# Optimization experiments

Hardware: AMD Instinct MI355X
Metric: run time of the kernel (lower is better)

The kernel has to match this reference:

```python
import jax, jax.numpy as jnp
import numpy as np

Nu, Nd = 40000, 20000          # users, drugs
FIN, HID, H = 128, 256, 4      # input feat, hidden_dim, heads
D = HID // H                   # per-head dim (64)
HAN_OUT, HD = 64, 16           # HANConv out_channels, per-head dim
E, ER = 80000, 80000           # edges per relation (main / refined graph)


def _seg_softmax(a, seg, num):
    # segment softmax over destination index, stable
    m = jax.ops.segment_max(a, seg, num_segments=num)
    ex = jnp.exp(a - m[seg])
    s = jax.ops.segment_sum(ex, seg, num_segments=num)
    return ex / (s[seg] + 1e-16)


def setup_inputs():
    key = jax.random.key(0)
    ks = iter(jax.random.split(key, 80))
    def nrm(shape, scale=0.05):
        return jax.random.normal(next(ks), shape, jnp.float32) * scale
    def edges(ns, nd, e):
        src = jax.random.randint(next(ks), (e,), 0, ns)
        dst = jax.random.randint(next(ks), (e,), 0, nd)
        return jnp.stack([src, dst]).astype(jnp.int32)
    return {
        'x_user': nrm((Nu, FIN), 1.0), 'x_drug': nrm((Nd, FIN), 1.0),
        'x_user_ref': nrm((Nu, FIN), 1.0),
        'ei_ud': edges(Nu, Nd, E), 'ei_du': edges(Nd, Nu, E), 'ei_uu': edges(Nu, Nu, E),
        'ei_r1': edges(Nu, Nu, ER), 'ei_r2': edges(Nu, Nu, ER),
        # HANConv params (refined graph, user-only)
        'W_han': nrm((FIN, HAN_OUT)), 'b_han': jnp.zeros((HAN_OUT,), jnp.float32),
        'a_src_r1': nrm((H, HD)), 'a_dst_r1': nrm((H, HD)),
        'a_src_r2': nrm((H, HD)), 'a_dst_r2': nrm((H, HD)),
        'Wk_sem': nrm((HAN_OUT, HAN_OUT)), 'bk_sem': jnp.zeros((HAN_OUT,), jnp.float32),
        'q_sem': nrm((HAN_OUT,)),
        # per-node-type input linears
        'W_in_user': nrm((FIN, HID)), 'b_in_user': jnp.zeros((HID,), jnp.float32),
        'W_in_drug': nrm((FIN, HID)), 'b_in_drug': jnp.zeros((HID,), jnp.float32),
        # HGTConv params
        'W_kqv_user': nrm((HID, 3 * HID)), 'b_kqv_user': jnp.zeros((3 * HID,), jnp.float32),
        'W_kqv_drug': nrm((HID, 3 * HID)), 'b_kqv_drug': jnp.zeros((3 * HID,), jnp.float32),
        'Wk_ud': nrm((H, D, D), 0.1), 'Wv_ud': nrm((H, D, D), 0.1), 'p_ud': jnp.ones((H,), jnp.float32),
        'Wk_du': nrm((H, D, D), 0.1), 'Wv_du': nrm((H, D, D), 0.1), 'p_du': jnp.ones((H,), jnp.float32),
        'Wk_uu': nrm((H, D, D), 0.1), 'Wv_uu': nrm((H, D, D), 0.1), 'p_uu': jnp.ones((H,), jnp.float32),
        'W_out_user': nrm((HID, HID)), 'b_out_user': jnp.zeros((HID,), jnp.float32),
        'W_out_drug': nrm((HID, HID)), 'b_out_drug': jnp.zeros((HID,), jnp.float32),
        'skip_user': jnp.array(1.0, jnp.float32), 'skip_drug': jnp.array(1.0, jnp.float32),
        # final fusion linear
        'W_fin': nrm((HID + HAN_OUT, HID)), 'b_fin': jnp.zeros((HID,), jnp.float32),
    }


def reference(x_user, x_drug, x_user_ref, ei_ud, ei_du, ei_uu, ei_r1, ei_r2,
              W_han, b_han, a_src_r1, a_dst_r1, a_src_r2, a_dst_r2,
              Wk_sem, bk_sem, q_sem,
              W_in_user, b_in_user, W_in_drug, b_in_drug,
              W_kqv_user, b_kqv_user, W_kqv_drug, b_kqv_drug,
              Wk_ud, Wv_ud, p_ud, Wk_du, Wv_du, p_du, Wk_uu, Wv_uu, p_uu,
              W_out_user, b_out_user, W_out_drug, b_out_drug,
              skip_user, skip_drug, W_fin, b_fin):
    # ---------- HANConv on refined graph (two user-user meta-paths) ----------
    h = (x_user_ref @ W_han + b_han).reshape(Nu, H, HD)
    outs = []
    for ei, a_s, a_d in ((ei_r1, a_src_r1, a_dst_r1), (ei_r2, a_src_r2, a_dst_r2)):
        s, d = ei[0], ei[1]
        al_s = (h * a_s).sum(-1)                      # [Nu,H]
        al_d = (h * a_d).sum(-1)
        al = jax.nn.leaky_relu(al_s[s] + al_d[d], 0.2)  # [ER,H]
        al = _seg_softmax(al, d, Nu)
        o = jax.ops.segment_sum(h[s] * al[:, :, None], d, num_segments=Nu)
        outs.append(jax.nn.relu(o.reshape(Nu, HAN_OUT)))
    outs = jnp.stack(outs)                            # [2,Nu,64]
    score = (q_sem * jnp.tanh(outs @ Wk_sem + bk_sem).mean(axis=1)).sum(-1)  # [2]
    sem = jax.nn.softmax(score, axis=0)
    x_ref_out = (sem[:, None, None] * outs).sum(0)    # [Nu,64]

    # ---------- per-node-type input projection + relu ----------
    xu = jax.nn.relu(x_user @ W_in_user + b_in_user)
    xd = jax.nn.relu(x_drug @ W_in_drug + b_in_drug)

    # ---------- HGTConv ----------
    kqv_u = xu @ W_kqv_user + b_kqv_user
    kqv_d = xd @ W_kqv_drug + b_kqv_drug
    ku, qu, vu = [t.reshape(-1, H, D) for t in jnp.split(kqv_u, 3, axis=1)]
    kd, qd, vd = [t.reshape(-1, H, D) for t in jnp.split(kqv_d, 3, axis=1)]
    q_all = jnp.concatenate([qu, qd], axis=0)         # dst offsets: user=0, drug=Nu
    src_feat = {'user': (ku, vu), 'drug': (kd, vd)}
    dst_off = {'user': 0, 'drug': Nu}
    edge_types = [('user', 'drug', ei_ud, Wk_ud, Wv_ud, p_ud),
                  ('drug', 'user', ei_du, Wk_du, Wv_du, p_du),
                  ('user', 'user', ei_uu, Wk_uu, Wv_uu, p_uu)]
    scale = 1.0 / np.sqrt(D).astype(np.float32)
    alphas, vals, dsts = [], [], []
    for st, dt, ei, Wk, Wv, p in edge_types:
        k_src, v_src = src_feat[st]
        kp = jnp.einsum('nhd,hde->nhe', k_src, Wk)    # relation-specific per-head transform
        vp = jnp.einsum('nhd,hde->nhe', v_src, Wv)
        s, d = ei[0], ei[1]
        gd = d + dst_off[dt]
        a = (q_all[gd] * kp[s]).sum(-1) * p[None, :] * scale  # [E,H]
        alphas.append(a); vals.append(vp[s]); dsts.append(gd)
    a = jnp.concatenate(alphas)
    v = jnp.concatenate(vals)
    gd = jnp.concatenate(dsts)
    a = _seg_softmax(a, gd, Nu + Nd)                  # softmax over all in-edges of each dst
    out = jax.ops.segment_sum(v * a[:, :, None], gd, num_segments=Nu + Nd)
    out = out.reshape(Nu + Nd, HID)
    ou, od = out[:Nu], out[Nu:]
    ou = jax.nn.gelu(ou, approximate=False) @ W_out_user + b_out_user
    od = jax.nn.gelu(od, approximate=False) @ W_out_drug + b_out_drug
    su = jax.nn.sigmoid(skip_user)
    sd = jax.nn.sigmoid(skip_drug)
    ou = su * ou + (1.0 - su) * xu
    od = sd * od + (1.0 - sd) * xd                    # drug branch (kept for fidelity)
    # ---------- fuse HGT user embedding with HAN refined embedding ----------
    x_emb = jnp.concatenate([ou, x_ref_out], axis=1) @ W_fin + b_fin
    return x_emb
```

## Files before the change

### kernel.cpp

```cpp
#include <hip/hip_runtime.h>
#include <hip/hip_bf16.h>

#define NU 40000
#define ND 20000
#define NUP 40192
#define NDP 20224
#define HIDC 256
#define NHEAD 4
#define NEDGE 80000
#define CHUNK 2048
#define NCH 20
#define AL4 (NU * 4)

typedef __attribute__((ext_vector_type(8))) short bf16x8;
typedef __attribute__((ext_vector_type(8))) unsigned short u16x8;
typedef __attribute__((ext_vector_type(4))) float f32x4;

static __device__ __forceinline__ float b2f(unsigned short u) {
  union { unsigned int u; float f; } x; x.u = (unsigned int)u << 16; return x.f;
}
static __device__ __forceinline__ unsigned short f2b(float f) {
  union { float f; unsigned int u; } x; x.f = f;
  unsigned int r = x.u + 0x7FFFu + ((x.u >> 16) & 1u);
  return (unsigned short)(r >> 16);
}

static __device__ __forceinline__ void gload_lds16(const void* g, void* l) {
  __builtin_amdgcn_global_load_lds((const __attribute__((address_space(1))) unsigned int*)g,
                                   (__attribute__((address_space(3))) unsigned int*)l, 16, 0, 0);
}

template<int ACT>
__global__ __launch_bounds__(512)
void gemm_bf16(const unsigned short* __restrict__ A,
               const unsigned short* __restrict__ Bt,
               const float* __restrict__ bias,
               float* __restrict__ Cf, int ldcf,
               unsigned short* __restrict__ Cb, int ldcb,
               int M, int N, int K, int Mblk,
               const float* __restrict__ skipp,
               const unsigned short* __restrict__ xprev,
               int halfRows,
               const unsigned short* __restrict__ Bt2,
               const float* __restrict__ bias2, int M2,
               const float* __restrict__ as1, const float* __restrict__ ad1,
               const float* __restrict__ as2, const float* __restrict__ ad2,
               float* __restrict__ alsd,
               int B1,
               const unsigned short* __restrict__ A_r2,
               const unsigned short* __restrict__ Bt_r2,
               const float* __restrict__ bias_r2,
               unsigned short* __restrict__ Cb_r2, int ldcb_r2,
               int M_r2, int N_r2, int Mblk_r2)
{
  __shared__ __attribute__((aligned(128))) unsigned char smem[49152];
  unsigned short* ldsA = (unsigned short*)smem;
  unsigned short* ldsB = ldsA + 16384;
  float* ldsE = (float*)smem;

  int flat = blockIdx.x;
  const unsigned short* Ap = A;
  const unsigned short* Btp = Bt;
  const float* biasp = bias;
  float* Cfp = Cf;
  unsigned short* Cbp = Cb;
  int ldcbp = ldcb, Mp = M, Np = N, Mblkp = Mblk;
  if (flat >= B1) {
    flat -= B1;
    Ap = A_r2; Btp = Bt_r2; biasp = bias_r2; Cbp = Cb_r2; ldcbp = ldcb_r2;
    Mp = M_r2; Np = N_r2; Mblkp = Mblk_r2; Cfp = nullptr;
  }

  const int Nx = (Np + 127) >> 7;
  const int S = Nx << 3;
  const int jj = flat % S, kq = flat / S;
  const int bx = jj >> 3, by = (kq << 3) + (jj & 7);
  if (by >= Mblkp) return;

  const int tid  = threadIdx.x;
  const int lane = tid & 63, wv = tid >> 6;
  const int row0 = by * 256, col0 = bx * 128;

  const unsigned short* Btu = Btp;
  const float* biasu = biasp;
  int Mu = Mp;
  int cfoff = 0;
  if (row0 >= halfRows) { Btu = Bt2; biasu = bias2; Mu = M2; cfoff = 64; }

  const int rl = lane >> 3;
  const int sS = (lane & 7) ^ rl;

  const int lr = lane & 15, lk = lane >> 4;
  const int wr = wv >> 1, wc = wv & 1;
  const int swz = lr & 7;

  f32x4 acc[4][4] = {};

  for (int k0 = 0; k0 < K; k0 += 64) {
#pragma unroll
    for (int i = 0; i < 4; i++) {
      size_t ga = (size_t)(row0 + wv * 32 + i * 8 + rl) * K + k0 + sS * 8;
      gload_lds16(Ap + ga, ldsA + wv * 2048 + i * 512);
    }
#pragma unroll
    for (int i = 0; i < 2; i++) {
      size_t gb = (size_t)(col0 + wv * 16 + i * 8 + rl) * K + k0 + sS * 8;
      gload_lds16(Btu + gb, ldsB + wv * 1024 + i * 512);
    }
    __syncthreads();
#pragma unroll
    for (int half = 0; half < 2; half++) {
      const int k8 = half * 4 + lk;
      const int so = (k8 ^ swz) << 3;
      bf16x8 av[4], bv[4];
#pragma unroll
      for (int m = 0; m < 4; m++)
        av[m] = *(const bf16x8*)&ldsA[(wr * 64 + m * 16 + lr) * 64 + so];
#pragma unroll
      for (int n = 0; n < 4; n++)
        bv[n] = *(const bf16x8*)&ldsB[(wc * 64 + n * 16 + lr) * 64 + so];
#pragma unroll
      for (int m = 0; m < 4; m++)
#pragma unroll
        for (int n = 0; n < 4; n++)
          acc[m][n] = __builtin_amdgcn_mfma_f32_16x16x32_bf16(av[m], bv[n], acc[m][n], 0, 0, 0);
    }
    __syncthreads();
  }

  if (ACT == 2) {
    __shared__ float csum[64];
    if (tid < 64) csum[tid] = 0.f;
    __syncthreads();
#pragma unroll
    for (int n = 0; n < 4; n++) {
      int col = col0 + wc * 64 + n * 16 + lr;
      if (col < Np) {
        float bi = biasu[col];
        float local = 0.f;
#pragma unroll
        for (int m = 0; m < 4; m++)
#pragma unroll
          for (int g = 0; g < 4; g++) {
            int row = row0 + wr * 64 + m * 16 + lk * 4 + g;
            if (row < Mu) local += tanhf(acc[m][n][g] + bi);
          }
        atomicAdd(&csum[col], local);
      }
    }
    __syncthreads();
    if (tid < 64) atomicAdd(&Cfp[cfoff + tid], csum[tid]);
    return;
  }

  float su = 0.f;
  if (ACT == 3) su = 1.f / (1.f + expf(-skipp[0]));
  float bi[4];
#pragma unroll
  for (int n = 0; n < 4; n++) {
    int col = col0 + wc * 64 + n * 16 + lr;
    bi[n] = (col < Np) ? biasu[col] : 0.f;
  }

#pragma unroll
  for (int ch = 0; ch < 4; ch++) {
    __syncthreads();
    if (wr == ch) {
#pragma unroll
      for (int m = 0; m < 4; m++)
#pragma unroll
        for (int n = 0; n < 4; n++) {
          int c = wc * 64 + n * 16 + lr;
          int wbase = c + 2 * (c >> 5);
#pragma unroll
          for (int g = 0; g < 4; g++) {
            int lrow = m * 16 + lk * 4 + g;
            ldsE[lrow * 134 + wbase] = acc[m][n][g] + bi[n];
          }
        }
    }
    __syncthreads();
#pragma unroll
    for (int i = 0; i < 2; i++) {
      int c = tid + i * 512;
      int lrow = c >> 4, cc = c & 15;
      int row = row0 + ch * 64 + lrow;
      int colb = cc * 8;
      int base = lrow * 134 + 8 * cc + 2 * (cc >> 2);
      float v[8];
#pragma unroll
      for (int q2 = 0; q2 < 4; q2++) {
        float2 tv = *(const float2*)&ldsE[base + 2 * q2];
        v[2 * q2] = tv.x; v[2 * q2 + 1] = tv.y;
      }
      if (ACT == 1) {
#pragma unroll
        for (int q = 0; q < 8; q++) v[q] = fmaxf(v[q], 0.f);
      }
      if (ACT == 3) {
        u16x8 xp = *(const u16x8*)(xprev + (size_t)row * 256 + col0 + colb);
#pragma unroll
        for (int q = 0; q < 8; q++) v[q] = su * v[q] + (1.f - su) * b2f(xp[q]);
      }
      if (ACT == 4) {
        if (colb < 64 && row < Mu) {
          int hh = colb >> 4;
          int o0 = colb & 15;
          float s1 = 0, d1 = 0, s2 = 0, d2 = 0;
#pragma unroll
          for (int q = 0; q < 8; q++) {
            float x = v[q];
            s1 += x * as1[hh * 16 + o0 + q];
            d1 += x * ad1[hh * 16 + o0 + q];
            s2 += x * as2[hh * 16 + o0 + q];
            d2 += x * ad2[hh * 16 + o0 + q];
          }
          s1 += __shfl_xor(s1, 1); d1 += __shfl_xor(d1, 1);
          s2 += __shfl_xor(s2, 1); d2 += __shfl_xor(d2, 1);
          if ((lane & 1) == 0) {
            size_t idx = (size_t)row * 4 + hh;
            alsd[idx]           = s1;
            alsd[AL4 + idx]     = d1;
            alsd[2 * AL4 + idx] = s2;
            alsd[3 * AL4 + idx] = d2;
          }
        }
      }
      if (Cbp) {
        int col = col0 + colb;
        if (col < Np) {
          u16x8 o;
#pragma unroll
          for (int q = 0; q < 8; q++) o[q] = f2b(row < Mu ? v[q] : 0.f);
          *(u16x8*)(Cbp + (size_t)row * ldcbp + col) = o;
        }
      }
      if (Cfp && row < Mu) {
        int col = col0 + colb;
        if (col < Np)
          *(float4*)&Cfp[(size_t)row * ldcf + col] = make_float4(v[0], v[1], v[2], v[3]);
        if (col + 4 < Np)
          *(float4*)&Cfp[(size_t)row * ldcf + col + 4] = make_float4(v[4], v[5], v[6], v[7]);
      }
    }
  }
}

__global__ __launch_bounds__(256)
void prep_all(const float* __restrict__ x_user, const float* __restrict__ x_drug,
              const float* __restrict__ x_user_ref,
              const float* __restrict__ W_in_user, const float* __restrict__ W_in_drug,
              const float* __restrict__ W_kqv_user, const float* __restrict__ W_kqv_drug,
              const float* __restrict__ W_out_user, const float* __restrict__ W_fin,
              const float* __restrict__ W_han, const float* __restrict__ Wk_sem,
              const float* __restrict__ Wk_uu, const float* __restrict__ Wv_uu,
              const float* __restrict__ Wk_du, const float* __restrict__ Wv_du,
              const float* __restrict__ b_kqv_user, const float* __restrict__ b_kqv_drug,
              unsigned short* __restrict__ xub, unsigned short* __restrict__ xdb,
              unsigned short* __restrict__ xrb,
              unsigned short* __restrict__ Btu_in, unsigned short* __restrict__ Btd_in,
              unsigned short* __restrict__ Btall_u, unsigned short* __restrict__ Btall_d,
              unsigned short* __restrict__ Bto, unsigned short* __restrict__ Btf,
              unsigned short* __restrict__ Bth, unsigned short* __restrict__ BtWk,
              float* __restrict__ ball_u, float* __restrict__ ball_d,
              int* __restrict__ cnt)
{
  __shared__ float sWh[4096];
  __shared__ float sWk[64][65];
  const int b = blockIdx.x;
  const int tid = threadIdx.x;

  if (b < 16) {
    int mat = b >> 2, hh = b & 3;
    const float* Wkqv; const float* Wh; unsigned short* Bt; int coloff;
    switch (mat) {
      case 0:  Wkqv = W_kqv_user; Wh = Wk_uu; Bt = Btall_u;          coloff = 0;   break;
      case 1:  Wkqv = W_kqv_user; Wh = Wv_uu; Bt = Btall_u + 131072; coloff = 512; break;
      case 2:  Wkqv = W_kqv_drug; Wh = Wk_du; Bt = Btall_d;          coloff = 0;   break;
      default: Wkqv = W_kqv_drug; Wh = Wv_du; Bt = Btall_d + 65536;  coloff = 512; break;
    }
    for (int i = tid; i < 4096; i += 256) sWh[i] = Wh[hh * 4096 + i];
    __syncthreads();
    for (int ct = 0; ct < 4; ct++) {
      for (int i = tid; i < 4096; i += 256) {
        int cl = i >> 6, d = i & 63;
        sWk[cl][d] = Wkqv[(size_t)(ct * 64 + cl) * 768 + coloff + hh * 64 + d];
      }
      __syncthreads();
      int cl = tid & 63, eg = tid >> 6;
      float acc[16] = {};
      for (int d = 0; d < 64; d++) {
        float w = sWk[cl][d];
#pragma unroll
        for (int e = 0; e < 16; e++) acc[e] += w * sWh[d * 64 + eg * 16 + e];
      }
#pragma unroll
      for (int e = 0; e < 16; e++)
        Bt[(size_t)(hh * 64 + eg * 16 + e) * 256 + ct * 64 + cl] = f2b(acc[e]);
      __syncthreads();
    }
    return;
  }
  if (b < 21) {
    int j = (b - 16) * 256 + tid;
    const float* bb; const float* Wh; float* outp; int coloff, e256;
    if (j < 256)       { outp = &ball_u[j];        bb = b_kqv_user; Wh = Wk_uu; coloff = 0;   e256 = j; }
    else if (j < 512)  { ball_u[j] = b_kqv_user[j]; return; }
    else if (j < 768)  { outp = &ball_u[j];        bb = b_kqv_user; Wh = Wv_uu; coloff = 512; e256 = j - 512; }
    else if (j < 1024) { outp = &ball_d[j - 768];  bb = b_kqv_drug; Wh = Wk_du; coloff = 0;   e256 = j - 768; }
    else               { outp = &ball_d[j - 768];  bb = b_kqv_drug; Wh = Wv_du; coloff = 512; e256 = j - 1024; }
    int hh = e256 >> 6, e = e256 & 63;
    float acc = 0.f;
    for (int d = 0; d < 64; d++)
      acc += bb[coloff + hh * 64 + d] * Wh[hh * 4096 + d * 64 + e];
    *outp = acc;
    return;
  }
  if (b < 139) {
    int u = (b - 21) * 256 + tid;
    int idx = u * 4;
    if (idx < 3 * NU) *(int4*)&cnt[idx] = make_int4(0, 0, 0, 0);
    return;
  }
  if (b < 1323) {
    size_t i = (size_t)(b - 139) * 256 + tid;
    const float* W; unsigned short* Bt; int ldw, coloff, K, N;
    if (i < 32768)       { W = W_in_user;  Bt = Btu_in;          ldw = 256; coloff = 0;   K = 128; N = 256; }
    else if (i < 65536)  { W = W_in_drug;  Bt = Btd_in;          ldw = 256; coloff = 0;   K = 128; N = 256; i -= 32768; }
    else if (i < 131072) { W = W_kqv_user; Bt = Btall_u + 65536; ldw = 768; coloff = 256; K = 256; N = 256; i -= 65536; }
    else if (i < 196608) { W = W_out_user; Bt = Bto;             ldw = 256; coloff = 0;   K = 256; N = 256; i -= 131072; }
    else if (i < 278528) { W = W_fin;      Bt = Btf;             ldw = 256; coloff = 0;   K = 320; N = 256; i -= 196608; }
    else if (i < 294912) { W = W_han;      Bt = Bth;             ldw = 64;  coloff = 0;   K = 128; N = 64;  i -= 278528; }
    else                 { W = Wk_sem;     Bt = BtWk;            ldw = 64;  coloff = 0;   K = 64;  N = 64;  i -= 294912; }
    int n = (int)(i / K), k = (int)(i - (size_t)n * K);
    Bt[i] = (n < N) ? f2b(W[(size_t)k * ldw + coloff + n]) : 0;
    return;
  }
  {
    int bc = b - 1323;
    const float* in; unsigned short* outp; int M; int bl;
    if (bc < 2512)      { in = x_user;     outp = xub; M = NU; bl = bc; }
    else if (bc < 3776) { in = x_drug;     outp = xdb; M = ND; bl = bc - 2512; }
    else                { in = x_user_ref; outp = xrb; M = NU; bl = bc - 3776; }
    size_t e0 = ((size_t)bl * 256 + tid) * 8;
    int r = (int)(e0 >> 7);
    u16x8 o;
    if (r < M) {
      float4 a = *(const float4*)(in + e0);
      float4 bb = *(const float4*)(in + e0 + 4);
      o[0] = f2b(a.x); o[1] = f2b(a.y); o[2] = f2b(a.z); o[3] = f2b(a.w);
      o[4] = f2b(bb.x); o[5] = f2b(bb.y); o[6] = f2b(bb.z); o[7] = f2b(bb.w);
    } else {
#pragma unroll
      for (int q = 0; q < 8; q++) o[q] = 0;
    }
    *(u16x8*)(outp + e0) = o;
  }
}

__global__ void hist_all(const int* __restrict__ ei_du, const int* __restrict__ ei_uu,
                         const int* __restrict__ ei_r1, const int* __restrict__ ei_r2,
                         int* __restrict__ cnt)
{
  int t = blockIdx.x * 256 + threadIdx.x;
  if (t >= NEDGE) return;
  const int* ei; int* c;
  switch (blockIdx.y) {
    case 0: ei = ei_du; c = cnt; break;
    case 1: ei = ei_uu; c = cnt; break;
    case 2: ei = ei_r1; c = cnt + NU; break;
    default: ei = ei_r2; c = cnt + 2 * NU; break;
  }
  atomicAdd(&c[ei[NEDGE + t]], 1);
}

__global__ __launch_bounds__(256)
void scan_partial(const int* __restrict__ cnt, int* __restrict__ csums)
{
  int b = blockIdx.x;
  int rel = b / NCH, ch = b - rel * NCH;
  const int* c = cnt + (size_t)rel * NU;
  int t = threadIdx.x;
  int i0 = ch * CHUNK + t * 8;
  int s = 0;
#pragma unroll
  for (int j = 0; j < 8; j++) { int i = i0 + j; if (i < NU) s += c[i]; }
  __shared__ int ps[256];
  ps[t] = s;
  __syncthreads();
  for (int d = 128; d > 0; d >>= 1) { if (t < d) ps[t] += ps[t + d]; __syncthreads(); }
  if (t == 0) csums[b] = ps[0];
}

__global__ void scan_mid(const int* __restrict__ csums, int* __restrict__ coffs,
                         int* __restrict__ rs, float* __restrict__ colpart2)
{
  int r = threadIdx.x;
  if (r < 128) colpart2[r] = 0.f;
  if (r >= 3) return;
  int run = 0;
  for (int ch = 0; ch < NCH; ch++) { coffs[r * NCH + ch] = run; run += csums[r * NCH + ch]; }
  rs[(size_t)r * NUP + NU] = run;
}

__global__ __launch_bounds__(256)
void scan_final(int* __restrict__ cnt, const int* __restrict__ coffs,
                int* __restrict__ rs)
{
  int b = blockIdx.x;
  int rel = b / NCH, ch = b - rel * NCH;
  int* c = cnt + (size_t)rel * NU;
  int* r = rs + (size_t)rel * NUP;
  int t = threadIdx.x;
  int i0 = ch * CHUNK + t * 8;
  int loc[8]; int s = 0;
#pragma unroll
  for (int j = 0; j < 8; j++) {
    int i = i0 + j;
    loc[j] = (i < NU) ? c[i] : 0;
    if (i < NU) c[i] = 0;
    s += loc[j];
  }
  __shared__ int ps[256];
  ps[t] = s;
  __syncthreads();
  for (int d = 1; d < 256; d <<= 1) {
    int o = (t >= d) ? ps[t - d] : 0;
    __syncthreads();
    ps[t] += o;
    __syncthreads();
  }
  int run = coffs[b] + ps[t] - s;
#pragma unroll
  for (int j = 0; j < 8; j++) { int i = i0 + j; if (i < NU) { r[i] = run; run += loc[j]; } }
}

__global__ void fill_all(const int* __restrict__ ei_r1, const int* __restrict__ ei_r2,
                         const int* __restrict__ ei_du, const int* __restrict__ ei_uu,
                         const float* __restrict__ alsd,
                         const unsigned short* __restrict__ qb,
                         const unsigned short* __restrict__ kvdb,
                         const float* __restrict__ p_du, const float* __restrict__ p_uu,
                         const int* __restrict__ rs, int* __restrict__ cur,
                         int* __restrict__ esrc1, float* __restrict__ aev1,
                         int* __restrict__ esrc2, float* __restrict__ aev2,
                         int* __restrict__ esrcH, float* __restrict__ aevH)
{
  int t = blockIdx.x * 256 + threadIdx.x;
  if (t >= NEDGE * 4) return;
  int y = blockIdx.y;
  int e = t >> 2, hh = t & 3;
  if (y < 2) {
    const int* ei = y ? ei_r2 : ei_r1;
    const float* als = alsd + (y ? 2 * AL4 : 0);
    const float* ald = alsd + (y ? 3 * AL4 : AL4);
    const int* rsp = rs + (size_t)(y ? 2 : 1) * NUP;
    int* curp = cur + (size_t)(y ? 2 : 1) * NU;
    int* esrc = y ? esrc2 : esrc1;
    float* aev = y ? aev2 : aev1;
    int s = ei[e], d = ei[NEDGE + e];
    float al = als[s * 4 + hh] + ald[d * 4 + hh];
    al = (al >= 0.f) ? al : 0.2f * al;
    float ex = expf(al);
    int pos = 0;
    if (hh == 0) pos = rsp[d] + atomicAdd(&curp[d], 1);
    pos = __shfl(pos, (threadIdx.x & 63) & ~3, 64);
    aev[pos * 4 + hh] = ex;
    if (hh == 0) esrc[pos] = s;
  } else {
    int yy = y - 2;
    const int* ei = yy ? ei_uu : ei_du;
    const unsigned short* kb = yy ? qb : kvdb;
    const int ks = yy ? 768 : 512;
    const int voff = yy ? 512 : NUP * 768 + 256;
    const float* p = yy ? p_uu : p_du;
    int s = ei[e], d = ei[NEDGE + e];
    const uint4* qv = (const uint4*)(qb + (size_t)d * 768 + 256 + hh * 64);
    const uint4* kv = (const uint4*)(kb + (size_t)s * ks + hh * 64);
    float acc = 0.f;
#pragma unroll
    for (int i = 0; i < 8; i++) {
      uint4 a = qv[i], b = kv[i];
      unsigned int aw[4] = {a.x, a.y, a.z, a.w};
      unsigned int bw[4] = {b.x, b.y, b.z, b.w};
#pragma unroll
      for (int u = 0; u < 4; u++) {
        acc += b2f((unsigned short)(aw[u] & 0xffff)) * b2f((unsigned short)(bw[u] & 0xffff));
        acc += b2f((unsigned short)(aw[u] >> 16))    * b2f((unsigned short)(bw[u] >> 16));
      }
    }
    float ex = expf(acc * p[hh] * 0.125f);
    int pos = 0;
    if (hh == 0) pos = rs[d] + atomicAdd(&cur[d], 1);
    pos = __shfl(pos, (threadIdx.x & 63) & ~3, 64);
    aevH[pos * 4 + hh] = ex;
    if (hh == 0) esrcH[pos] = voff + s * ks;
  }
}

__global__ __launch_bounds__(256)
void gather_all(const int* __restrict__ rs,
                const int* __restrict__ esrc1, const float* __restrict__ aev1,
                const int* __restrict__ esrc2, const float* __restrict__ aev2,
                const int* __restrict__ esrcH, const float* __restrict__ aevH,
                const unsigned short* __restrict__ hb,
                const unsigned short* __restrict__ vbase,
                unsigned short* __restrict__ obf1, unsigned short* __restrict__ obf2,
                unsigned short* __restrict__ houtb)
{
  int gid = blockIdx.x * 256 + threadIdx.x;
  int wid = gid >> 6, lane = gid & 63;
  if (wid >= NUP) return;
  int y = blockIdx.y;
  int head = lane >> 4;
  if (y < 2) {
    const int* rsp = rs + (size_t)(y ? 2 : 1) * NUP;
    const int* esrc = y ? esrc2 : esrc1;
    const float* aev = y ? aev2 : aev1;
    unsigned short* obf = y ? obf2 : obf1;
    int beg = 0, end = 0;
    if (wid < NU) { beg = rsp[wid]; end = rsp[wid + 1]; }
    float asum = 0.f, a = 0.f;
    for (int i0 = beg; i0 < end; i0 += 4) {
      int idx[4]; float w[4];
#pragma unroll
      for (int u = 0; u < 4; u++) {
        int i = i0 + u;
        int ic = (i < end) ? i : (end - 1);
        idx[u] = esrc[ic];
        float wv = aev[ic * 4 + head];
        w[u] = (i < end) ? wv : 0.f;
      }
      float hv[4];
#pragma unroll
      for (int u = 0; u < 4; u++)
        hv[u] = b2f(hb[(size_t)idx[u] * 64 + lane]);
#pragma unroll
      for (int u = 0; u < 4; u++) { asum += w[u]; a += w[u] * hv[u]; }
    }
    a *= 1.f / (asum + 1e-16f);
    obf[(size_t)wid * 64 + lane] = f2b(fmaxf(a, 0.f));
  } else {
    int beg = 0, end = 0;
    if (wid < NU) { beg = rs[wid]; end = rs[wid + 1]; }
    float asum = 0.f;
    float a0 = 0, a1 = 0, a2 = 0, a3 = 0;
    for (int i0 = beg; i0 < end; i0 += 4) {
      int idx[4]; float w[4];
#pragma unroll
      for (int u = 0; u < 4; u++) {
        int i = i0 + u;
        int ic = (i < end) ? i : (end - 1);
        idx[u] = esrcH[ic];
        float wv = aevH[ic * 4 + head];
        w[u] = (i < end) ? wv : 0.f;
      }
      ushort4 vv[4];
#pragma unroll
      for (int u = 0; u < 4; u++)
        vv[u] = *(const ushort4*)(vbase + (size_t)idx[u] + lane * 4);
#pragma unroll
      for (int u = 0; u < 4; u++) {
        asum += w[u];
        a0 += b2f(vv[u].x) * w[u]; a1 += b2f(vv[u].y) * w[u];
        a2 += b2f(vv[u].z) * w[u]; a3 += b2f(vv[u].w) * w[u];
      }
    }
    float inv = 1.f / (asum + 1e-16f);
    a0 *= inv; a1 *= inv; a2 *= inv; a3 *= inv;
    ushort4 o;
    o.x = f2b(0.5f * a0 * (1.f + erff(a0 * 0.70710678118654752f)));
    o.y = f2b(0.5f * a1 * (1.f + erff(a1 * 0.70710678118654752f)));
    o.z = f2b(0.5f * a2 * (1.f + erff(a2 * 0.70710678118654752f)));
    o.w = f2b(0.5f * a3 * (1.f + erff(a3 * 0.70710678118654752f)));
    *(ushort4*)(houtb + (size_t)wid * 256 + lane * 4) = o;
  }
}

__global__ void sem_final2(const float* __restrict__ colpart2,
                           const float* __restrict__ q_sem, float* __restrict__ semv)
{
  int t = threadIdx.x;
  int j = t & 63;
  __shared__ float sv[128];
  sv[t] = colpart2[t] * q_sem[j] * (1.0f / NU);
  __syncthreads();
  if (t == 0) {
    float s0 = 0, s1 = 0;
    for (int i = 0; i < 64; i++) { s0 += sv[i]; s1 += sv[64 + i]; }
    float m = fmaxf(s0, s1);
    float e0 = expf(s0 - m), e1 = expf(s1 - m);
    semv[0] = e0 / (e0 + e1); semv[1] = e1 / (e0 + e1);
  }
}

__global__ void fill_ref_b(const unsigned short* __restrict__ obf1,
                           const unsigned short* __restrict__ obf2,
                           const float* __restrict__ semv, unsigned short* __restrict__ afinb)
{
  int t = blockIdx.x * 256 + threadIdx.x;
  if (t >= NUP * 64) return;
  int n = t >> 6, j = t & 63;
  float v = semv[0] * b2f(obf1[t]) + semv[1] * b2f(obf2[t]);
  afinb[(size_t)n * 320 + 256 + j] = f2b(v);
}

extern "C" void kernel_launch(void* const* d_in, const int* in_sizes, int n_in,
                              void* d_out, int out_size, void* d_ws, size_t ws_size,
                              hipStream_t stream)
{
  (void)in_sizes; (void)n_in; (void)out_size; (void)ws_size;
  const float* x_user     = (const float*)d_in[0];
  const float* x_drug     = (const float*)d_in[1];
  const float* x_user_ref = (const float*)d_in[2];
  const int*   ei_du      = (const int*)d_in[4];
  const int*   ei_uu      = (const int*)d_in[5];
  const int*   ei_r1      = (const int*)d_in[6];
  const int*   ei_r2      = (const int*)d_in[7];
  const float* W_han      = (const float*)d_in[8];
  const float* b_han      = (const float*)d_in[9];
  const float* a_src_r1   = (const float*)d_in[10];
  const float* a_dst_r1   = (const float*)d_in[11];
  const float* a_src_r2   = (const float*)d_in[12];
  const float* a_dst_r2   = (const float*)d_in[13];
  const float* Wk_sem     = (const float*)d_in[14];
  const float* bk_sem     = (const float*)d_in[15];
  const float* q_sem      = (const float*)d_in[16];
  const float* W_in_user  = (const float*)d_in[17];
  const float* b_in_user  = (const float*)d_in[18];
  const float* W_in_drug  = (const float*)d_in[19];
  const float* b_in_drug  = (const float*)d_in[20];
  const float* W_kqv_user = (const float*)d_in[21];
  const float* b_kqv_user = (const float*)d_in[22];
  const float* W_kqv_drug = (const float*)d_in[23];
  const float* b_kqv_drug = (const float*)d_in[24];
  const float* Wk_du      = (const float*)d_in[28];
  const float* Wv_du      = (const float*)d_in[29];
  const float* p_du       = (const float*)d_in[30];
  const float* Wk_uu      = (const float*)d_in[31];
  const float* Wv_uu      = (const float*)d_in[32];
  const float* p_uu       = (const float*)d_in[33];
  const float* W_out_user = (const float*)d_in[34];
  const float* b_out_user = (const float*)d_in[35];
  const float* skip_user  = (const float*)d_in[38];
  const float* W_fin      = (const float*)d_in[40];
  const float* b_fin      = (const float*)d_in[41];
  float* out = (float*)d_out;

  char* base = (char*)d_ws;
  size_t off = 0;
  auto alloc = [&](size_t bytes) { char* p = base + off; off += (bytes + 255) & ~(size_t)255; return p; };

  unsigned short* hb = (unsigned short*)alloc((size_t)NUP * 64 * 2);
  float* alsd    = (float*)alloc((size_t)4 * AL4 * 4);
  float* colpart2= (float*)alloc(128 * 4);
  float* semv    = (float*)alloc(64);
  float* ball_u  = (float*)alloc(768 * 4);
  float* ball_d  = (float*)alloc(512 * 4);

  int* cnt   = (int*)alloc((size_t)3 * NU * 4);
  int* rs    = (int*)alloc((size_t)3 * NUP * 4);
  int* csums = (int*)alloc((size_t)3 * NCH * 4);
  int* coffs = (int*)alloc((size_t)3 * NCH * 4);
  int* esrcH = (int*)alloc((size_t)2 * NEDGE * 4);
  float* aevH= (float*)alloc((size_t)2 * NEDGE * 4 * 4);
  int* esrc1 = (int*)alloc((size_t)NEDGE * 4);
  float* aev1= (float*)alloc((size_t)NEDGE * 4 * 4);
  int* esrc2 = (int*)alloc((size_t)NEDGE * 4);
  float* aev2= (float*)alloc((size_t)NEDGE * 4 * 4);

  unsigned short* obf1 = (unsigned short*)alloc((size_t)NUP * 64 * 2);
  unsigned short* obf2 = (unsigned short*)alloc((size_t)NUP * 64 * 2);

  unsigned short* qukvb = (unsigned short*)alloc((size_t)NUP * 768 * 2);
  unsigned short* kvdb  = (unsigned short*)alloc((size_t)NDP * 512 * 2);

  unsigned short* xub2d = (unsigned short*)alloc((size_t)NUP * 256 * 2);
  unsigned short* xdb2d = (unsigned short*)alloc((size_t)NDP * 256 * 2);

  unsigned short* houtb = (unsigned short*)alloc((size_t)NUP * 256 * 2);
  unsigned short* xrb   = houtb;

  unsigned short* afinb = (unsigned short*)alloc((size_t)NUP * 320 * 2);
  unsigned short* xub   = afinb;
  unsigned short* xdb   = afinb + (size_t)NUP * 128;

  unsigned short* Btu_in  = (unsigned short*)alloc(256 * 128 * 2);
  unsigned short* Btd_in  = (unsigned short*)alloc(256 * 128 * 2);
  unsigned short* Btall_u = (unsigned short*)alloc(768 * 256 * 2);
  unsigned short* Btall_d = (unsigned short*)alloc(512 * 256 * 2);
  unsigned short* Bto     = (unsigned short*)alloc(256 * 256 * 2);
  unsigned short* Btf     = (unsigned short*)alloc(256 * 320 * 2);
  unsigned short* Bth     = (unsigned short*)alloc(128 * 128 * 2);
  unsigned short* BtWk    = (unsigned short*)alloc(128 * 64 * 2);

  dim3 blk(256), blk5(512);
  auto g1 = [](size_t n) { return dim3((unsigned)((n + 255) / 256)); };
  auto gg = [](int N, int Mblk) {
    int Nx = (N + 127) / 128;
    return (unsigned)(((Mblk + 7) / 8) * 8 * Nx);
  };
  const int BIG = 1 << 30;
  const unsigned short* NB = nullptr;
  const float* NF = nullptr;
  unsigned short* NBm = nullptr;

  const int prep_blocks = 16 + 5 + 118 + 1184 + 6288;
  prep_all<<<dim3(prep_blocks), blk, 0, stream>>>(
      x_user, x_drug, x_user_ref, W_in_user, W_in_drug, W_kqv_user, W_kqv_drug,
      W_out_user, W_fin, W_han, Wk_sem, Wk_uu, Wv_uu, Wk_du, Wv_du,
      b_kqv_user, b_kqv_drug,
      xub, xdb, xrb, Btu_in, Btd_in, Btall_u, Btall_d, Bto, Btf, Bth, BtWk,
      ball_u, ball_d, cnt);

  hist_all<<<dim3((NEDGE + 255) / 256, 4), blk, 0, stream>>>(ei_du, ei_uu, ei_r1, ei_r2, cnt);
  scan_partial<<<3 * NCH, blk, 0, stream>>>(cnt, csums);
  scan_mid<<<1, 128, 0, stream>>>(csums, coffs, rs, colpart2);
  scan_final<<<3 * NCH, blk, 0, stream>>>(cnt, coffs, rs);

  gemm_bf16<4><<<gg(64, 157), blk5, 0, stream>>>(
      xrb, Bth, b_han, (float*)nullptr, 0, hb, 64, NU, 64, 128, 157,
      nullptr, nullptr, BIG, NB, NF, 0,
      a_src_r1, a_dst_r1, a_src_r2, a_dst_r2, alsd,
      BIG, NB, NB, NF, NBm, 0, 0, 0, 0);

  gemm_bf16<1><<<gg(256, 236), blk5, 0, stream>>>(
      xub, Btu_in, b_in_user, (float*)nullptr, 0, xub2d, 256, NU, 256, 128, 236,
      nullptr, nullptr, NUP, Btd_in, b_in_drug, NUP + ND,
      NF, NF, NF, NF, nullptr,
      BIG, NB, NB, NF, NBm, 0, 0, 0, 0);

  {
    unsigned B1 = gg(768, 157), B2 = gg(512, 79);
    gemm_bf16<0><<<dim3(B1 + B2), blk5, 0, stream>>>(
        xub2d, Btall_u, ball_u, (float*)nullptr, 0, qukvb, 768, NU, 768, 256, 157,
        nullptr, nullptr, BIG, NB, NF, 0, NF, NF, NF, NF, nullptr,
        (int)B1, xdb2d, Btall_d, ball_d, kvdb, 512, ND, 512, 79);
  }

  fill_all<<<dim3((NEDGE * 4 + 255) / 256, 4), blk, 0, stream>>>(
      ei_r1, ei_r2, ei_du, ei_uu, alsd, qukvb, kvdb, p_du, p_uu,
      rs, cnt, esrc1, aev1, esrc2, aev2, esrcH, aevH);

  gather_all<<<dim3((NUP * 64 + 255) / 256, 3), blk, 0, stream>>>(
      rs, esrc1, aev1, esrc2, aev2, esrcH, aevH, hb, qukvb, obf1, obf2, houtb);

  gemm_bf16<2><<<gg(64, 314), blk5, 0, stream>>>(
      obf1, BtWk, bk_sem, colpart2, 0, NBm, 0, NU, 64, 64, 314,
      nullptr, nullptr, NUP, BtWk, bk_sem, NUP + NU,
      NF, NF, NF, NF, nullptr,
      BIG, NB, NB, NF, NBm, 0, 0, 0, 0);
  sem_final2<<<1, 128, 0, stream>>>(colpart2, q_sem, semv);

  gemm_bf16<3><<<gg(256, 157), blk5, 0, stream>>>(
      houtb, Bto, b_out_user, (float*)nullptr, 0, afinb, 320, NU, 256, 256, 157,
      skip_user, xub2d, BIG, NB, NF, 0, NF, NF, NF, NF, nullptr,
      BIG, NB, NB, NF, NBm, 0, 0, 0, 0);
  fill_ref_b<<<g1((size_t)NUP * 64), blk, 0, stream>>>(obf1, obf2, semv, afinb);

  gemm_bf16<0><<<gg(256, 157), blk5, 0, stream>>>(
      afinb, Btf, b_fin, out, 256, NBm, 0, NU, 256, 320, 157,
      nullptr, nullptr, BIG, NB, NF, 0, NF, NF, NF, NF, nullptr,
      BIG, NB, NB, NF, NBm, 0, 0, 0, 0);
}
```

Before: 259.4 us.

## Move HGT attention score computation from edge fill into destination gather

The q·k dot products and exp for the HGT relations are no longer computed per edge in fill_all and stored to aevH. Instead, gather_all loads the destination's query once, reads each neighbour's key alongside its value, reduces the dot product with 16-lane shuffles, and applies exp on the fly. The source-type flag is packed into the low bit of the stored offset. This removes the aevH buffer and its write/read traffic, and makes fill_all's HGT branch one thread per edge, at the cost of extra key loads and shuffle work inside the gather loop.

```diff
diff --git a/kernel.cpp b/kernel.cpp
--- a/kernel.cpp
+++ b/kernel.cpp
@@ -438,13 +438,10 @@
 __global__ void fill_all(const int* __restrict__ ei_r1, const int* __restrict__ ei_r2,
                          const int* __restrict__ ei_du, const int* __restrict__ ei_uu,
                          const float* __restrict__ alsd,
-                         const unsigned short* __restrict__ qb,
-                         const unsigned short* __restrict__ kvdb,
-                         const float* __restrict__ p_du, const float* __restrict__ p_uu,
                          const int* __restrict__ rs, int* __restrict__ cur,
                          int* __restrict__ esrc1, float* __restrict__ aev1,
                          int* __restrict__ esrc2, float* __restrict__ aev2,
-                         int* __restrict__ esrcH, float* __restrict__ aevH)
+                         int* __restrict__ esrcH)
 {
   int t = blockIdx.x * 256 + threadIdx.x;
   if (t >= NEDGE * 4) return;
@@ -468,33 +465,13 @@
     aev[pos * 4 + hh] = ex;
     if (hh == 0) esrc[pos] = s;
   } else {
+    if (hh != 0) return;
     int yy = y - 2;
     const int* ei = yy ? ei_uu : ei_du;
-    const unsigned short* kb = yy ? qb : kvdb;
-    const int ks = yy ? 768 : 512;
-    const int voff = yy ? 512 : NUP * 768 + 256;
-    const float* p = yy ? p_uu : p_du;
     int s = ei[e], d = ei[NEDGE + e];
-    const uint4* qv = (const uint4*)(qb + (size_t)d * 768 + 256 + hh * 64);
-    const uint4* kv = (const uint4*)(kb + (size_t)s * ks + hh * 64);
-    float acc = 0.f;
-#pragma unroll
-    for (int i = 0; i < 8; i++) {
-      uint4 a = qv[i], b = kv[i];
-      unsigned int aw[4] = {a.x, a.y, a.z, a.w};
-      unsigned int bw[4] = {b.x, b.y, b.z, b.w};
-#pragma unroll
-      for (int u = 0; u < 4; u++) {
-        acc += b2f((unsigned short)(aw[u] & 0xffff)) * b2f((unsigned short)(bw[u] & 0xffff));
-        acc += b2f((unsigned short)(aw[u] >> 16))    * b2f((unsigned short)(bw[u] >> 16));
-      }
-    }
-    float ex = expf(acc * p[hh] * 0.125f);
-    int pos = 0;
-    if (hh == 0) pos = rs[d] + atomicAdd(&cur[d], 1);
-    pos = __shfl(pos, (threadIdx.x & 63) & ~3, 64);
-    aevH[pos * 4 + hh] = ex;
-    if (hh == 0) esrcH[pos] = voff + s * ks;
+    int pos = rs[d] + atomicAdd(&cur[d], 1);
+    int kb = yy ? ((s * 768) | 1) : (NUP * 768 + s * 512);
+    esrcH[pos] = kb;
   }
 }
 
@@ -502,9 +479,10 @@
 void gather_all(const int* __restrict__ rs,
                 const int* __restrict__ esrc1, const float* __restrict__ aev1,
                 const int* __restrict__ esrc2, const float* __restrict__ aev2,
-                const int* __restrict__ esrcH, const float* __restrict__ aevH,
+                const int* __restrict__ esrcH,
                 const unsigned short* __restrict__ hb,
                 const unsigned short* __restrict__ vbase,
+                const float* __restrict__ p_du, const float* __restrict__ p_uu,
                 unsigned short* __restrict__ obf1, unsigned short* __restrict__ obf2,
                 unsigned short* __restrict__ houtb)
 {
@@ -543,27 +521,41 @@
   } else {
     int beg = 0, end = 0;
     if (wid < NU) { beg = rs[wid]; end = rs[wid + 1]; }
+    ushort4 qv = *(const ushort4*)(vbase + (size_t)wid * 768 + 256 + lane * 4);
+    float q0 = b2f(qv.x), q1 = b2f(qv.y), q2 = b2f(qv.z), q3 = b2f(qv.w);
+    float pd = p_du[head] * 0.125f, pu = p_uu[head] * 0.125f;
     float asum = 0.f;
     float a0 = 0, a1 = 0, a2 = 0, a3 = 0;
     for (int i0 = beg; i0 < end; i0 += 4) {
-      int idx[4]; float w[4];
+      int kb[4]; int live[4];
 #pragma unroll
       for (int u = 0; u < 4; u++) {
         int i = i0 + u;
         int ic = (i < end) ? i : (end - 1);
-        idx[u] = esrcH[ic];
-        float wv = aevH[ic * 4 + head];
-        w[u] = (i < end) ? wv : 0.f;
-      }
-      ushort4 vv[4];
-#pragma unroll
-      for (int u = 0; u < 4; u++)
-        vv[u] = *(const ushort4*)(vbase + (size_t)idx[u] + lane * 4);
+        kb[u] = esrcH[ic];
+        live[u] = (i < end) ? 1 : 0;
+      }
+      ushort4 kk[4], vv[4];
 #pragma unroll
       for (int u = 0; u < 4; u++) {
-        asum += w[u];
-        a0 += b2f(vv[u].x) * w[u]; a1 += b2f(vv[u].y) * w[u];
-        a2 += b2f(vv[u].z) * w[u]; a3 += b2f(vv[u].w) * w[u];
+        int base = kb[u] & ~1;
+        int type = kb[u] & 1;
+        kk[u] = *(const ushort4*)(vbase + (size_t)base + lane * 4);
+        vv[u] = *(const ushort4*)(vbase + (size_t)(base + 256 + 256 * type) + lane * 4);
+      }
+#pragma unroll
+      for (int u = 0; u < 4; u++) {
+        float part = q0 * b2f(kk[u].x) + q1 * b2f(kk[u].y)
+                   + q2 * b2f(kk[u].z) + q3 * b2f(kk[u].w);
+        part += __shfl_xor(part, 1, 16);
+        part += __shfl_xor(part, 2, 16);
+        part += __shfl_xor(part, 4, 16);
+        part += __shfl_xor(part, 8, 16);
+        float pp = (kb[u] & 1) ? pu : pd;
+        float w = live[u] ? expf(part * pp) : 0.f;
+        asum += w;
+        a0 += b2f(vv[u].x) * w; a1 += b2f(vv[u].y) * w;
+        a2 += b2f(vv[u].z) * w; a3 += b2f(vv[u].w) * w;
       }
     }
     float inv = 1.f / (asum + 1e-16f);
@@ -663,7 +655,6 @@
   int* csums = (int*)alloc((size_t)3 * NCH * 4);
   int* coffs = (int*)alloc((size_t)3 * NCH * 4);
   int* esrcH = (int*)alloc((size_t)2 * NEDGE * 4);
-  float* aevH= (float*)alloc((size_t)2 * NEDGE * 4 * 4);
   int* esrc1 = (int*)alloc((size_t)NEDGE * 4);
   float* aev1= (float*)alloc((size_t)NEDGE * 4 * 4);
   int* esrc2 = (int*)alloc((size_t)NEDGE * 4);
@@ -739,11 +730,12 @@
   }
 
   fill_all<<<dim3((NEDGE * 4 + 255) / 256, 4), blk, 0, stream>>>(
-      ei_r1, ei_r2, ei_du, ei_uu, alsd, qukvb, kvdb, p_du, p_uu,
-      rs, cnt, esrc1, aev1, esrc2, aev2, esrcH, aevH);
+      ei_r1, ei_r2, ei_du, ei_uu, alsd,
+      rs, cnt, esrc1, aev1, esrc2, aev2, esrcH);
 
   gather_all<<<dim3((NUP * 64 + 255) / 256, 3), blk, 0, stream>>>(
-      rs, esrc1, aev1, esrc2, aev2, esrcH, aevH, hb, qukvb, obf1, obf2, houtb);
+      rs, esrc1, aev1, esrc2, aev2, esrcH, hb, qukvb, p_du, p_uu,
+      obf1, obf2, houtb);
 
   gemm_bf16<2><<<gg(64, 314), blk5, 0, stream>>>(
       obf1, BtWk, bk_sem, colpart2, 0, NBm, 0, NU, 64, 64, 314,
```

Result: faster. 248.4 us, median of 2 (-4.3%).
